# Kernel optimization log

Measured on AMD Instinct MI355X. Metric: run time of the kernel, lower is better.

## Reference

```python
import jax, jax.numpy as jnp
import numpy as np

# Fixed multi-scale geometry implied by the module's hard-coded reshapes
# (48^2=2304, 24^2=576, 12^2=144; Len_q = 576).
SPATIAL = [(48, 48), (24, 24), (12, 12)]
NH, NP, NL = 6, 4, 3  # num_heads, num_points, num_levels


def _process_reference_points(rp):
    """rp: (B, 3024, 2) normalized refs over 3 levels -> (B, 576, 2).
    Mirrors the part1/part2/part3 averaging in MSDeformAttn.forward."""
    B = rp.shape[0]
    p1 = rp[:, :2304].reshape(B, 48, 48, 2).mean(axis=(1, 2))[:, None, :]
    p1 = jnp.broadcast_to(p1, (B, 576, 2))
    p2 = rp[:, 2304:2880].reshape(B, 576, 2)
    p3 = rp[:, 2880:].reshape(B, 12, 12, 2)
    p3 = jax.image.resize(p3, (B, 24, 24, 2), 'bilinear')  # align_corners=False
    p3 = p3.reshape(B, 576, 2)
    return (p1 + p2 + p3) / 3.0


def _bilinear_sample(val_l, coords, Hl, Wl):
    """val_l: (B, Hl*Wl, nh, d) one level's values.
    coords: (B, Lq, nh, P, 2) normalized (x, y) sampling locations.
    Returns (B, Lq, P, nh, d) bilinearly sampled values (zero padding)."""
    B, Lq, nh, P, _ = coords.shape
    px = coords[..., 0] * Wl - 0.5
    py = coords[..., 1] * Hl - 0.5
    x0 = jnp.floor(px)
    y0 = jnp.floor(py)
    lx = px - x0
    ly = py - y0
    x0i = x0.astype(jnp.int32)
    y0i = y0.astype(jnp.int32)

    def _flat(a):  # (B,Lq,nh,P) -> (B,Lq*P,nh,1) matching value layout
        return a.transpose(0, 1, 3, 2).reshape(B, Lq * P, nh, 1)

    def gather(xi, yi):
        valid = (xi >= 0) & (xi < Wl) & (yi >= 0) & (yi < Hl)
        xi_c = jnp.clip(xi, 0, Wl - 1)
        yi_c = jnp.clip(yi, 0, Hl - 1)
        idx = _flat(yi_c * Wl + xi_c)
        v = jnp.take_along_axis(val_l, idx, axis=1)  # (B,Lq*P,nh,d)
        return v * _flat(valid).astype(val_l.dtype)

    w00 = _flat((1 - lx) * (1 - ly))
    w10 = _flat(lx * (1 - ly))
    w01 = _flat((1 - lx) * ly)
    w11 = _flat(lx * ly)
    out = (gather(x0i, y0i) * w00 + gather(x0i + 1, y0i) * w10 +
           gather(x0i, y0i + 1) * w01 + gather(x0i + 1, y0i + 1) * w11)
    return out.reshape(B, Lq, P, nh, -1)


def setup_inputs() -> dict:
    key = jax.random.key(0)
    ks = jax.random.split(key, 8)
    B, C = 32, 384
    Lq, Lv = 576, 3024
    # reference points exactly as get_reference_points builds them
    refs = []
    for (Hl, Wl) in SPATIAL:
        ry, rx = np.meshgrid(np.linspace(0.5, Hl - 0.5, Hl) / Hl,
                             np.linspace(0.5, Wl - 0.5, Wl) / Wl, indexing='ij')
        refs.append(np.stack([rx.ravel(), ry.ravel()], -1))
    rp = np.concatenate(refs, 0).astype(np.float32)  # (3024, 2)
    rp = np.broadcast_to(rp[None, :, None, :], (B, Lv, 1, 2)).copy()
    s = 1.0 / np.sqrt(C)
    return {
        'query': jax.random.normal(ks[0], (B, Lq, C), jnp.float32),
        'value': jax.random.normal(ks[1], (B, Lv, C), jnp.float32),
        'reference_points': jnp.asarray(rp),
        'W_value': jax.random.normal(ks[2], (C, C), jnp.float32) * s,
        'b_value': jnp.zeros((C,), jnp.float32),
        'W_off': jax.random.normal(ks[3], (C, NH * NL * NP * 2), jnp.float32) * 0.01,
        'b_off': jnp.zeros((NH * NL * NP * 2,), jnp.float32),
        'W_attn': jax.random.normal(ks[4], (C, NH * NL * NP), jnp.float32) * s,
        'b_attn': jnp.zeros((NH * NL * NP,), jnp.float32),
        'W_out': jax.random.normal(ks[5], (C, C), jnp.float32) * s,
        'b_out': jnp.zeros((C,), jnp.float32),
    }


def reference(query, value, reference_points, W_value, b_value, W_off, b_off,
              W_attn, b_attn, W_out, b_out):
    B, Lq, C = query.shape
    d = C // NH
    val = (value @ W_value + b_value).reshape(B, -1, NH, d)
    off = (query @ W_off + b_off).reshape(B, Lq, NH, NL, NP, 2)
    attn = jax.nn.softmax((query @ W_attn + b_attn)
                          .reshape(B, Lq, NH, NL * NP), axis=-1)
    attn = attn.reshape(B, Lq, NH, NL, NP)
    ref = _process_reference_points(reference_points.reshape(B, -1, 2))
    coords = off + ref[:, :, None, None, None, :]  # (B,Lq,nh,L,P,2)
    out = jnp.zeros((B, Lq, NH, d), query.dtype)
    start = 0
    for l, (Hl, Wl) in enumerate(SPATIAL):
        val_l = val[:, start:start + Hl * Wl]
        sampled = _bilinear_sample(val_l, coords[:, :, :, l], Hl, Wl)
        out = out + jnp.einsum('bqpnd,bqnp->bqnd', sampled, attn[:, :, :, l])
        start += Hl * Wl
    return out.reshape(B, Lq, NH * d) @ W_out + b_out
```

## Files before the change

kernel.cpp:

```cpp
#include <hip/hip_runtime.h>
#include <cmath>

#define B_SZ   32
#define LQ     576
#define LV     3024
#define CDIM   384
#define NHEAD  6
#define DHEAD  64
#define NLVL   3
#define NPTS   4
#define NPROJ  216
#define NPROJP 256

typedef short    bx4 __attribute__((ext_vector_type(4)));
typedef short    bx8 __attribute__((ext_vector_type(8)));
typedef float    fx4 __attribute__((ext_vector_type(4)));
typedef _Float16 hx8 __attribute__((ext_vector_type(8)));

__device__ __forceinline__ short f2bf(float f) {
    unsigned u = __builtin_bit_cast(unsigned, f);
    unsigned r = (u + 0x7FFFu + ((u >> 16) & 1u)) >> 16;
    return (short)r;
}
__device__ __forceinline__ float bf2f(unsigned short u) {
    return __builtin_bit_cast(float, ((unsigned)u) << 16);
}
__device__ __forceinline__ short f2h(float f) {
    return __builtin_bit_cast(short, (_Float16)f);
}

__global__ __launch_bounds__(256) void cast_transpose_kernel(
    const float* __restrict__ W, short* __restrict__ Wt, int K, int N)
{
    int idx = blockIdx.x * 256 + threadIdx.x;
    if (idx >= K * N) return;
    int n = idx / K, k = idx - n * K;
    Wt[idx] = f2bf(W[(size_t)k * N + n]);
}

__global__ __launch_bounds__(256) void prep_proj_f16_kernel(
    const float* __restrict__ W_off, const float* __restrict__ b_off,
    const float* __restrict__ W_attn, const float* __restrict__ b_attn,
    short* __restrict__ Wf, float* __restrict__ bc)
{
    int idx = blockIdx.x * 256 + threadIdx.x;
    if (idx >= NPROJP * CDIM) return;
    int n = idx / CDIM, k = idx - n * CDIM;
    float w = 0.f;
    if (n < 144)           w = W_off[(size_t)k * 144 + n];
    else if (n < NPROJ)    w = W_attn[(size_t)k * 72 + (n - 144)];
    Wf[idx] = f2h(w);
    if (idx < NPROJP)
        bc[idx] = (idx < 144) ? b_off[idx]
                 : (idx < NPROJ ? b_attn[idx - 144] : 0.f);
}

__global__ __launch_bounds__(256) void value_gemm_kernel(
    const float* __restrict__ A, const short* __restrict__ Bt,
    const float* __restrict__ bias, short* __restrict__ Cout,
    int M, int K)
{
    constexpr int N = 384;
    __shared__ short As[2][64 * 64];
    __shared__ short Bs[2][192 * 64];

    const int tid = threadIdx.x;
    const int m0 = blockIdx.x * 64;
    const int n0 = blockIdx.y * 192;

    const int w  = tid >> 6;
    const int l  = tid & 63;
    const int wc = w * 48;
    const int lr = l & 15;
    const int q  = l >> 4;

    const int rg  = l >> 3;
    const int cg  = l & 7;
    const int csw = cg ^ rg;

    const int ar   = tid >> 4;
    const int kq   = (tid & 15) << 2;
    const int oct  = kq >> 3;
    const int koff = kq & 7;
    const int aswz = ((oct ^ (ar & 7)) << 3) + koff;
    const float* gA0 = A + (size_t)(m0 + ar) * K + kq;

    fx4 acc[4][3] = {};
    float4 v0, v1, v2, v3;

    auto issueB = [&](int buf, int t) {
        #pragma unroll
        for (int u = 0; u < 6; ++u) {
            const int rbase = w * 48 + u * 8;
            const short* gB = Bt + (size_t)(n0 + rbase + rg) * K + t * 64 + csw * 8;
            __builtin_amdgcn_global_load_lds(
                (const __attribute__((address_space(1))) void*)gB,
                (__attribute__((address_space(3))) void*)&Bs[buf][rbase * 64],
                16, 0, 0);
        }
    };
    auto loadA = [&](int t) {
        const float* g = gA0 + t * 64;
        v0 = *(const float4*)(g);
        v1 = *(const float4*)(g + (size_t)16 * K);
        v2 = *(const float4*)(g + (size_t)32 * K);
        v3 = *(const float4*)(g + (size_t)48 * K);
    };
    auto writeA = [&](int buf) {
        bx4 s;
        s[0]=f2bf(v0.x); s[1]=f2bf(v0.y); s[2]=f2bf(v0.z); s[3]=f2bf(v0.w);
        *(bx4*)&As[buf][(ar +  0) * 64 + aswz] = s;
        s[0]=f2bf(v1.x); s[1]=f2bf(v1.y); s[2]=f2bf(v1.z); s[3]=f2bf(v1.w);
        *(bx4*)&As[buf][(ar + 16) * 64 + aswz] = s;
        s[0]=f2bf(v2.x); s[1]=f2bf(v2.y); s[2]=f2bf(v2.z); s[3]=f2bf(v2.w);
        *(bx4*)&As[buf][(ar + 32) * 64 + aswz] = s;
        s[0]=f2bf(v3.x); s[1]=f2bf(v3.y); s[2]=f2bf(v3.z); s[3]=f2bf(v3.w);
        *(bx4*)&As[buf][(ar + 48) * 64 + aswz] = s;
    };

    issueB(0, 0);
    loadA(0);
    writeA(0);
    __syncthreads();

    #pragma unroll
    for (int t = 0; t < 6; ++t) {
        const int cur = t & 1;

        if (t < 5) { loadA(t + 1); issueB(cur ^ 1, t + 1); }

        #pragma unroll
        for (int ks = 0; ks < 2; ++ks) {
            bx8 af[4], bf[3];
            #pragma unroll
            for (int i = 0; i < 4; ++i)
                af[i] = *(const bx8*)&As[cur][(i * 16 + lr) * 64 +
                                             (((ks * 4 + q) ^ (lr & 7)) << 3)];
            #pragma unroll
            for (int j = 0; j < 3; ++j)
                bf[j] = *(const bx8*)&Bs[cur][(wc + j * 16 + lr) * 64 +
                                             (((ks * 4 + q) ^ (lr & 7)) << 3)];
            #pragma unroll
            for (int i = 0; i < 4; ++i)
                #pragma unroll
                for (int j = 0; j < 3; ++j)
                    acc[i][j] = __builtin_amdgcn_mfma_f32_16x16x32_bf16(
                        af[i], bf[j], acc[i][j], 0, 0, 0);
        }

        if (t < 5) writeA(cur ^ 1);

        __syncthreads();
    }

    float bv[3];
    #pragma unroll
    for (int j = 0; j < 3; ++j) bv[j] = bias[n0 + wc + j * 16 + lr];
    const int rrow = q * 4;
    #pragma unroll
    for (int i = 0; i < 4; ++i) {
        #pragma unroll
        for (int r = 0; r < 4; ++r) {
            const int row = m0 + i * 16 + rrow + r;
            #pragma unroll
            for (int j = 0; j < 3; ++j) {
                const int col = n0 + wc + j * 16 + lr;
                Cout[(size_t)row * N + col] = f2bf(acc[i][j][r] + bv[j]);
            }
        }
    }
}

template <bool OUT_BF16>
__global__ __launch_bounds__(256) void gemm_dma_kernel(
    const short* __restrict__ A, const short* __restrict__ Bt,
    const float* __restrict__ bias, void* __restrict__ Cout,
    int M, int K)
{
    constexpr int N = 384;
    __shared__ short As[128 * 64];
    __shared__ short Bs[128 * 64];

    const int tid = threadIdx.x;
    const int n0 = blockIdx.x * 128;
    const int m0 = blockIdx.y * 128;

    const int w  = tid >> 6;
    const int l  = tid & 63;
    const int wr = (w & 1) * 64;
    const int wc = (w >> 1) * 64;
    const int lr = l & 15;
    const int q  = l >> 4;

    const int rg  = l >> 3;
    const int cg  = l & 7;
    const int csw = cg ^ rg;

    fx4 acc[4][4] = {};

    for (int k0 = 0; k0 < K; k0 += 64) {
        #pragma unroll
        for (int t = 0; t < 4; ++t) {
            const int rbase = w * 32 + t * 8;
            const short* gA = A + (size_t)(m0 + rbase + rg) * K + k0 + csw * 8;
            __builtin_amdgcn_global_load_lds(
                (const __attribute__((address_space(1))) void*)gA,
                (__attribute__((address_space(3))) void*)&As[rbase * 64],
                16, 0, 0);
            const short* gB = Bt + (size_t)(n0 + rbase + rg) * K + k0 + csw * 8;
            __builtin_amdgcn_global_load_lds(
                (const __attribute__((address_space(1))) void*)gB,
                (__attribute__((address_space(3))) void*)&Bs[rbase * 64],
                16, 0, 0);
        }
        __syncthreads();

        #pragma unroll
        for (int ks = 0; ks < 2; ++ks) {
            bx8 af[4], bf[4];
            #pragma unroll
            for (int i = 0; i < 4; ++i)
                af[i] = *(const bx8*)&As[(wr + i * 16 + lr) * 64 +
                                         (((ks * 4 + q) ^ (lr & 7)) << 3)];
            #pragma unroll
            for (int j = 0; j < 4; ++j)
                bf[j] = *(const bx8*)&Bs[(wc + j * 16 + lr) * 64 +
                                         (((ks * 4 + q) ^ (lr & 7)) << 3)];
            #pragma unroll
            for (int i = 0; i < 4; ++i)
                #pragma unroll
                for (int j = 0; j < 4; ++j)
                    acc[i][j] = __builtin_amdgcn_mfma_f32_16x16x32_bf16(
                        af[i], bf[j], acc[i][j], 0, 0, 0);
        }
        __syncthreads();
    }

    const int rrow = q * 4;
    #pragma unroll
    for (int j = 0; j < 4; ++j) {
        const int col = n0 + wc + j * 16 + lr;
        const float bv = bias[col];
        #pragma unroll
        for (int i = 0; i < 4; ++i) {
            const int row = m0 + wr + i * 16 + rrow;
            #pragma unroll
            for (int r = 0; r < 4; ++r) {
                if (OUT_BF16)
                    ((short*)Cout)[(size_t)(row + r) * N + col] = f2bf(acc[i][j][r] + bv);
                else
                    ((float*)Cout)[(size_t)(row + r) * N + col] = acc[i][j][r] + bv;
            }
        }
    }
}

__global__ __launch_bounds__(256) void gemm_proj_kernel(
    const float* __restrict__ A, const short* __restrict__ Wf,
    const float* __restrict__ bias, float* __restrict__ C,
    int M, int K)
{
    __shared__ short As[128 * 72];
    __shared__ short Bs[128 * 72];

    const int tid = threadIdx.x;
    const int n0 = blockIdx.x * 128;
    const int m0 = blockIdx.y * 128;

    const int w  = tid >> 6;
    const int l  = tid & 63;
    const int wr = (w & 1) * 64;
    const int wc = (w >> 1) * 64;
    const int lr = l & 15;
    const int ko = (l >> 4) * 8;

    fx4 acc[4][4] = {};

    for (int k0 = 0; k0 < K; k0 += 64) {
        #pragma unroll
        for (int r = 0; r < 8; ++r) {
            const int id = tid + r * 256;
            const int m  = id >> 4;
            const int kq = (id & 15) << 2;
            const float4 v = *(const float4*)(A + (size_t)(m0 + m) * K + k0 + kq);
            bx4 s;
            s[0] = f2h(v.x); s[1] = f2h(v.y); s[2] = f2h(v.z); s[3] = f2h(v.w);
            *(bx4*)&As[m * 72 + kq] = s;
        }
        #pragma unroll
        for (int r = 0; r < 4; ++r) {
            const int id = tid + r * 256;
            const int n  = id >> 3;
            const int k8 = (id & 7) << 3;
            *(bx8*)&Bs[n * 72 + k8] = *(const bx8*)(Wf + (size_t)(n0 + n) * K + k0 + k8);
        }
        __syncthreads();

        #pragma unroll
        for (int ks = 0; ks < 2; ++ks) {
            bx8 af[4], bf[4];
            #pragma unroll
            for (int i = 0; i < 4; ++i)
                af[i] = *(const bx8*)&As[(wr + i * 16 + lr) * 72 + ks * 32 + ko];
            #pragma unroll
            for (int j = 0; j < 4; ++j)
                bf[j] = *(const bx8*)&Bs[(wc + j * 16 + lr) * 72 + ks * 32 + ko];
            #pragma unroll
            for (int i = 0; i < 4; ++i)
                #pragma unroll
                for (int j = 0; j < 4; ++j)
                    acc[i][j] = __builtin_amdgcn_mfma_f32_16x16x32_f16(
                        __builtin_bit_cast(hx8, af[i]),
                        __builtin_bit_cast(hx8, bf[j]), acc[i][j], 0, 0, 0);
        }
        __syncthreads();
    }

    const int rrow = (l >> 4) * 4;
    #pragma unroll
    for (int j = 0; j < 4; ++j) {
        const int col = n0 + wc + j * 16 + lr;
        if (col >= NPROJ) continue;
        const float bv = bias[col];
        #pragma unroll
        for (int i = 0; i < 4; ++i) {
            const int row = m0 + wr + i * 16 + rrow;
            #pragma unroll
            for (int r = 0; r < 4; ++r)
                C[(size_t)(row + r) * NPROJ + col] = acc[i][j][r] + bv;
        }
    }
}

__global__ __launch_bounds__(256) void ref_kernel(
    const float* __restrict__ rp, float* __restrict__ refp)
{
    const int b = blockIdx.x;
    const float* r = rp + (size_t)b * LV * 2;
    const int tid = threadIdx.x;

    __shared__ float redx[256], redy[256];
    float sx = 0.f, sy = 0.f;
    for (int i = tid; i < 2304; i += 256) {
        sx += r[2 * i + 0];
        sy += r[2 * i + 1];
    }
    redx[tid] = sx; redy[tid] = sy;
    __syncthreads();
    for (int s = 128; s > 0; s >>= 1) {
        if (tid < s) { redx[tid] += redx[tid + s]; redy[tid] += redy[tid + s]; }
        __syncthreads();
    }
    const float p1x = redx[0] * (1.f / 2304.f);
    const float p1y = redy[0] * (1.f / 2304.f);

    const float* g = r + 2880 * 2;
    for (int q = tid; q < 576; q += 256) {
        const float p2x = r[(2304 + q) * 2 + 0];
        const float p2y = r[(2304 + q) * 2 + 1];
        const int qy = q / 24, qx = q % 24;
        const float syc = fminf(fmaxf(0.5f * qy - 0.25f, 0.f), 11.f);
        const float sxc = fminf(fmaxf(0.5f * qx - 0.25f, 0.f), 11.f);
        int y0 = min((int)syc, 10);
        int x0 = min((int)sxc, 10);
        const float fy = syc - (float)y0, fx = sxc - (float)x0;
        const float v00x = g[(y0 * 12 + x0) * 2 + 0],     v00y = g[(y0 * 12 + x0) * 2 + 1];
        const float v10x = g[(y0 * 12 + x0 + 1) * 2 + 0], v10y = g[(y0 * 12 + x0 + 1) * 2 + 1];
        const float v01x = g[((y0 + 1) * 12 + x0) * 2 + 0],     v01y = g[((y0 + 1) * 12 + x0) * 2 + 1];
        const float v11x = g[((y0 + 1) * 12 + x0 + 1) * 2 + 0], v11y = g[((y0 + 1) * 12 + x0 + 1) * 2 + 1];
        const float p3x = (1.f - fy) * ((1.f - fx) * v00x + fx * v10x)
                        + fy * ((1.f - fx) * v01x + fx * v11x);
        const float p3y = (1.f - fy) * ((1.f - fx) * v00y + fx * v10y)
                        + fy * ((1.f - fx) * v01y + fx * v11y);
        refp[((size_t)b * LQ + q) * 2 + 0] = (p1x + p2x + p3x) * (1.f / 3.f);
        refp[((size_t)b * LQ + q) * 2 + 1] = (p1y + p2y + p3y) * (1.f / 3.f);
    }
}

__global__ __launch_bounds__(192) void sample_kernel(
    const unsigned short* __restrict__ val, const float* __restrict__ proj,
    const float* __restrict__ refp, unsigned* __restrict__ mid)
{
    const int i = blockIdx.x;
    const int g = i & 7;
    const int r = i >> 3;
    const int b = g * 4 + (r / LQ);
    const int q = r - (r / LQ) * LQ;
    const int bq = b * LQ + q;
    const int tid = threadIdx.x;

    __shared__ float attn[72];
    __shared__ int   sloc[72][4];
    __shared__ float swt[72][4];

    if (tid < 72) {
        attn[tid] = proj[(size_t)bq * NPROJ + 144 + tid];

        const int h = tid / 12;
        const int rr = tid % 12;
        const int l = rr >> 2;
        const int p = rr & 3;

        const int HL[3] = {48, 24, 12};
        const int ST[3] = {0, 2304, 2880};
        const int Hl = HL[l], Wl = HL[l], st = ST[l];

        const float rx = refp[bq * 2 + 0];
        const float ry = refp[bq * 2 + 1];
        const int oc = ((h * NLVL + l) * NPTS + p) * 2;
        const float cx = proj[(size_t)bq * NPROJ + oc + 0] + rx;
        const float cy = proj[(size_t)bq * NPROJ + oc + 1] + ry;

        const float px = cx * (float)Wl - 0.5f;
        const float py = cy * (float)Hl - 0.5f;
        const float x0f = floorf(px), y0f = floorf(py);
        const float lx = px - x0f, ly = py - y0f;
        const int x0 = (int)x0f, y0 = (int)y0f;

        #pragma unroll
        for (int k = 0; k < 4; ++k) {
            const int dx = k & 1, dy = k >> 1;
            const int xi = x0 + dx, yi = y0 + dy;
            const bool v = (xi >= 0) && (xi < Wl) && (yi >= 0) && (yi < Hl);
            const int xc = min(max(xi, 0), Wl - 1);
            const int yc = min(max(yi, 0), Hl - 1);
            sloc[tid][k] = st + yc * Wl + xc;
            const float wx = dx ? lx : 1.f - lx;
            const float wy = dy ? ly : 1.f - ly;
            swt[tid][k] = v ? wx * wy : 0.f;
        }
    }
    __syncthreads();

    if (tid < NHEAD) {
        float mx = -1e30f;
        #pragma unroll
        for (int j = 0; j < 12; ++j) mx = fmaxf(mx, attn[tid * 12 + j]);
        float s = 0.f;
        #pragma unroll
        for (int j = 0; j < 12; ++j) {
            const float e = expf(attn[tid * 12 + j] - mx);
            attn[tid * 12 + j] = e;
            s += e;
        }
        const float inv = 1.f / s;
        #pragma unroll
        for (int j = 0; j < 12; ++j) attn[tid * 12 + j] *= inv;
    }
    __syncthreads();

    const int h  = tid >> 5;
    const int c2 = (tid & 31) << 1;
    const unsigned* vp = (const unsigned*)(val + (size_t)b * LV * CDIM + h * DHEAD + c2);
    float acc0 = 0.f, acc1 = 0.f;
    #pragma unroll
    for (int s = 0; s < 12; ++s) {
        const int j = h * 12 + s;
        const float a = attn[j];
        float s0 = 0.f, s1 = 0.f;
        #pragma unroll
        for (int k = 0; k < 4; ++k) {
            const unsigned u = vp[(size_t)sloc[j][k] * (CDIM / 2)];
            const float lo = __builtin_bit_cast(float, u << 16);
            const float hi = __builtin_bit_cast(float, u & 0xFFFF0000u);
            s0 += swt[j][k] * lo;
            s1 += swt[j][k] * hi;
        }
        acc0 += a * s0;
        acc1 += a * s1;
    }
    const unsigned lo = (unsigned)(unsigned short)f2bf(acc0);
    const unsigned hi = (unsigned)(unsigned short)f2bf(acc1);
    mid[((size_t)bq * CDIM + h * DHEAD + c2) >> 1] = lo | (hi << 16);
}

extern "C" void kernel_launch(void* const* d_in, const int* in_sizes, int n_in,
                              void* d_out, int out_size, void* d_ws, size_t ws_size,
                              hipStream_t stream)
{
    (void)in_sizes; (void)n_in; (void)out_size; (void)ws_size;

    const float* query   = (const float*)d_in[0];
    const float* value   = (const float*)d_in[1];
    const float* rp      = (const float*)d_in[2];
    const float* W_value = (const float*)d_in[3];
    const float* b_value = (const float*)d_in[4];
    const float* W_off   = (const float*)d_in[5];
    const float* b_off   = (const float*)d_in[6];
    const float* W_attn  = (const float*)d_in[7];
    const float* b_attn  = (const float*)d_in[8];
    const float* W_out   = (const float*)d_in[9];
    const float* b_out   = (const float*)d_in[10];
    float* out = (float*)d_out;

    char* p = (char*)d_ws;
    auto take = [&](size_t bytes) { char* q = p; p += (bytes + 255) & ~(size_t)255; return q; };
    short* val  = (short*)take((size_t)B_SZ * LV * CDIM * 2);
    short* mid  = (short*)take((size_t)B_SZ * LQ * CDIM * 2);
    short* Wtv  = (short*)take((size_t)CDIM * CDIM * 2);
    short* Wto  = (short*)take((size_t)CDIM * CDIM * 2);
    short* Wf   = (short*)take((size_t)NPROJP * CDIM * 2);
    float* proj = (float*)take((size_t)B_SZ * LQ * NPROJ * 4);
    float* refp = (float*)take((size_t)B_SZ * LQ * 2 * 4);
    float* bc   = (float*)take((size_t)NPROJP * 4);

    const int Mv = B_SZ * LV;
    const int Mq = B_SZ * LQ;

    cast_transpose_kernel<<<(CDIM * CDIM + 255) / 256, 256, 0, stream>>>(
        W_value, Wtv, CDIM, CDIM);
    cast_transpose_kernel<<<(CDIM * CDIM + 255) / 256, 256, 0, stream>>>(
        W_out, Wto, CDIM, CDIM);
    prep_proj_f16_kernel<<<(NPROJP * CDIM + 255) / 256, 256, 0, stream>>>(
        W_off, b_off, W_attn, b_attn, Wf, bc);

    value_gemm_kernel<<<dim3(Mv / 64, 2), 256, 0, stream>>>(
        value, Wtv, b_value, val, Mv, CDIM);
    gemm_proj_kernel<<<dim3(2, Mq / 128), 256, 0, stream>>>(
        query, Wf, bc, proj, Mq, CDIM);
    ref_kernel<<<B_SZ, 256, 0, stream>>>(rp, refp);
    sample_kernel<<<Mq, 192, 0, stream>>>(
        (const unsigned short*)val, proj, refp, (unsigned*)mid);
    gemm_dma_kernel<false><<<dim3(3, Mq / 128), 256, 0, stream>>>(
        mid, Wto, b_out, out, Mq, CDIM);
}
```

Baseline: 391.7 us.

## Load GEMM B operands directly from global memory and merge weight-prep kernels

```diff
diff --git a/kernel.cpp b/kernel.cpp
--- a/kernel.cpp
+++ b/kernel.cpp
@@ -29,30 +29,33 @@
     return __builtin_bit_cast(short, (_Float16)f);
 }
 
-__global__ __launch_bounds__(256) void cast_transpose_kernel(
-    const float* __restrict__ W, short* __restrict__ Wt, int K, int N)
-{
-    int idx = blockIdx.x * 256 + threadIdx.x;
-    if (idx >= K * N) return;
-    int n = idx / K, k = idx - n * K;
-    Wt[idx] = f2bf(W[(size_t)k * N + n]);
-}
-
-__global__ __launch_bounds__(256) void prep_proj_f16_kernel(
+__global__ __launch_bounds__(256) void prep_all_kernel(
+    const float* __restrict__ W_value, const float* __restrict__ W_out,
     const float* __restrict__ W_off, const float* __restrict__ b_off,
     const float* __restrict__ W_attn, const float* __restrict__ b_attn,
+    short* __restrict__ Wtv, short* __restrict__ Wto,
     short* __restrict__ Wf, float* __restrict__ bc)
 {
-    int idx = blockIdx.x * 256 + threadIdx.x;
-    if (idx >= NPROJP * CDIM) return;
-    int n = idx / CDIM, k = idx - n * CDIM;
-    float w = 0.f;
-    if (n < 144)           w = W_off[(size_t)k * 144 + n];
-    else if (n < NPROJ)    w = W_attn[(size_t)k * 72 + (n - 144)];
-    Wf[idx] = f2h(w);
-    if (idx < NPROJP)
-        bc[idx] = (idx < 144) ? b_off[idx]
-                 : (idx < NPROJ ? b_attn[idx - 144] : 0.f);
+    const int idx = blockIdx.x * 256 + threadIdx.x;
+    constexpr int SQ = CDIM * CDIM;
+    if (idx < SQ) {
+        int n = idx / CDIM, k = idx - n * CDIM;
+        Wtv[idx] = f2bf(W_value[(size_t)k * CDIM + n]);
+    } else if (idx < 2 * SQ) {
+        int i = idx - SQ;
+        int n = i / CDIM, k = i - n * CDIM;
+        Wto[i] = f2bf(W_out[(size_t)k * CDIM + n]);
+    } else if (idx < 2 * SQ + NPROJP * CDIM) {
+        int i = idx - 2 * SQ;
+        int n = i / CDIM, k = i - n * CDIM;
+        float w = 0.f;
+        if (n < 144)        w = W_off[(size_t)k * 144 + n];
+        else if (n < NPROJ) w = W_attn[(size_t)k * 72 + (n - 144)];
+        Wf[i] = f2h(w);
+        if (i < NPROJP)
+            bc[i] = (i < 144) ? b_off[i]
+                   : (i < NPROJ ? b_attn[i - 144] : 0.f);
+    }
 }
 
 __global__ __launch_bounds__(256) void value_gemm_kernel(
@@ -62,7 +65,6 @@
 {
     constexpr int N = 384;
     __shared__ short As[2][64 * 64];
-    __shared__ short Bs[2][192 * 64];
 
     const int tid = threadIdx.x;
     const int m0 = blockIdx.x * 64;
@@ -73,10 +75,6 @@
     const int wc = w * 48;
     const int lr = l & 15;
     const int q  = l >> 4;
-
-    const int rg  = l >> 3;
-    const int cg  = l & 7;
-    const int csw = cg ^ rg;
 
     const int ar   = tid >> 4;
     const int kq   = (tid & 15) << 2;
@@ -85,20 +83,14 @@
     const int aswz = ((oct ^ (ar & 7)) << 3) + koff;
     const float* gA0 = A + (size_t)(m0 + ar) * K + kq;
 
+    const short* gB[3];
+    #pragma unroll
+    for (int j = 0; j < 3; ++j)
+        gB[j] = Bt + (size_t)(n0 + wc + j * 16 + lr) * K + q * 8;
+
     fx4 acc[4][3] = {};
     float4 v0, v1, v2, v3;
 
-    auto issueB = [&](int buf, int t) {
-        #pragma unroll
-        for (int u = 0; u < 6; ++u) {
-            const int rbase = w * 48 + u * 8;
-            const short* gB = Bt + (size_t)(n0 + rbase + rg) * K + t * 64 + csw * 8;
-            __builtin_amdgcn_global_load_lds(
-                (const __attribute__((address_space(1))) void*)gB,
-                (__attribute__((address_space(3))) void*)&Bs[buf][rbase * 64],
-                16, 0, 0);
-        }
-    };
     auto loadA = [&](int t) {
         const float* g = gA0 + t * 64;
         v0 = *(const float4*)(g);
@@ -118,7 +110,6 @@
         *(bx4*)&As[buf][(ar + 48) * 64 + aswz] = s;
     };
 
-    issueB(0, 0);
     loadA(0);
     writeA(0);
     __syncthreads();
@@ -127,7 +118,7 @@
     for (int t = 0; t < 6; ++t) {
         const int cur = t & 1;
 
-        if (t < 5) { loadA(t + 1); issueB(cur ^ 1, t + 1); }
+        if (t < 5) loadA(t + 1);
 
         #pragma unroll
         for (int ks = 0; ks < 2; ++ks) {
@@ -138,8 +129,7 @@
                                              (((ks * 4 + q) ^ (lr & 7)) << 3)];
             #pragma unroll
             for (int j = 0; j < 3; ++j)
-                bf[j] = *(const bx8*)&Bs[cur][(wc + j * 16 + lr) * 64 +
-                                             (((ks * 4 + q) ^ (lr & 7)) << 3)];
+                bf[j] = *(const bx8*)(gB[j] + t * 64 + ks * 32);
             #pragma unroll
             for (int i = 0; i < 4; ++i)
                 #pragma unroll
@@ -149,7 +139,6 @@
         }
 
         if (t < 5) writeA(cur ^ 1);
-
         __syncthreads();
     }
 
@@ -171,15 +160,13 @@
     }
 }
 
-template <bool OUT_BF16>
 __global__ __launch_bounds__(256) void gemm_dma_kernel(
     const short* __restrict__ A, const short* __restrict__ Bt,
-    const float* __restrict__ bias, void* __restrict__ Cout,
+    const float* __restrict__ bias, float* __restrict__ Cout,
     int M, int K)
 {
     constexpr int N = 384;
     __shared__ short As[128 * 64];
-    __shared__ short Bs[128 * 64];
 
     const int tid = threadIdx.x;
     const int n0 = blockIdx.x * 128;
@@ -195,6 +182,11 @@
     const int rg  = l >> 3;
     const int cg  = l & 7;
     const int csw = cg ^ rg;
+
+    const short* gB[4];
+    #pragma unroll
+    for (int j = 0; j < 4; ++j)
+        gB[j] = Bt + (size_t)(n0 + wc + j * 16 + lr) * K + q * 8;
 
     fx4 acc[4][4] = {};
 
@@ -207,11 +199,6 @@
                 (const __attribute__((address_space(1))) void*)gA,
                 (__attribute__((address_space(3))) void*)&As[rbase * 64],
                 16, 0, 0);
-            const short* gB = Bt + (size_t)(n0 + rbase + rg) * K + k0 + csw * 8;
-            __builtin_amdgcn_global_load_lds(
-                (const __attribute__((address_space(1))) void*)gB,
-                (__attribute__((address_space(3))) void*)&Bs[rbase * 64],
-                16, 0, 0);
         }
         __syncthreads();
 
@@ -224,8 +211,7 @@
                                          (((ks * 4 + q) ^ (lr & 7)) << 3)];
             #pragma unroll
             for (int j = 0; j < 4; ++j)
-                bf[j] = *(const bx8*)&Bs[(wc + j * 16 + lr) * 64 +
-                                         (((ks * 4 + q) ^ (lr & 7)) << 3)];
+                bf[j] = *(const bx8*)(gB[j] + k0 + ks * 32);
             #pragma unroll
             for (int i = 0; i < 4; ++i)
                 #pragma unroll
@@ -245,12 +231,8 @@
         for (int i = 0; i < 4; ++i) {
             const int row = m0 + wr + i * 16 + rrow;
             #pragma unroll
-            for (int r = 0; r < 4; ++r) {
-                if (OUT_BF16)
-                    ((short*)Cout)[(size_t)(row + r) * N + col] = f2bf(acc[i][j][r] + bv);
-                else
-                    ((float*)Cout)[(size_t)(row + r) * N + col] = acc[i][j][r] + bv;
-            }
+            for (int r = 0; r < 4; ++r)
+                Cout[(size_t)(row + r) * N + col] = acc[i][j][r] + bv;
         }
     }
 }
@@ -261,7 +243,6 @@
     int M, int K)
 {
     __shared__ short As[128 * 72];
-    __shared__ short Bs[128 * 72];
 
     const int tid = threadIdx.x;
     const int n0 = blockIdx.x * 128;
@@ -273,6 +254,11 @@
     const int wc = (w >> 1) * 64;
     const int lr = l & 15;
     const int ko = (l >> 4) * 8;
+
+    const short* gB[4];
+    #pragma unroll
+    for (int j = 0; j < 4; ++j)
+        gB[j] = Wf + (size_t)(n0 + wc + j * 16 + lr) * K + ko;
 
     fx4 acc[4][4] = {};
 
@@ -287,13 +273,6 @@
             s[0] = f2h(v.x); s[1] = f2h(v.y); s[2] = f2h(v.z); s[3] = f2h(v.w);
             *(bx4*)&As[m * 72 + kq] = s;
         }
-        #pragma unroll
-        for (int r = 0; r < 4; ++r) {
-            const int id = tid + r * 256;
-            const int n  = id >> 3;
-            const int k8 = (id & 7) << 3;
-            *(bx8*)&Bs[n * 72 + k8] = *(const bx8*)(Wf + (size_t)(n0 + n) * K + k0 + k8);
-        }
         __syncthreads();
 
         #pragma unroll
@@ -304,7 +283,7 @@
                 af[i] = *(const bx8*)&As[(wr + i * 16 + lr) * 72 + ks * 32 + ko];
             #pragma unroll
             for (int j = 0; j < 4; ++j)
-                bf[j] = *(const bx8*)&Bs[(wc + j * 16 + lr) * 72 + ks * 32 + ko];
+                bf[j] = *(const bx8*)(gB[j] + k0 + ks * 32);
             #pragma unroll
             for (int i = 0; i < 4; ++i)
                 #pragma unroll
@@ -507,12 +486,9 @@
     const int Mv = B_SZ * LV;
     const int Mq = B_SZ * LQ;
 
-    cast_transpose_kernel<<<(CDIM * CDIM + 255) / 256, 256, 0, stream>>>(
-        W_value, Wtv, CDIM, CDIM);
-    cast_transpose_kernel<<<(CDIM * CDIM + 255) / 256, 256, 0, stream>>>(
-        W_out, Wto, CDIM, CDIM);
-    prep_proj_f16_kernel<<<(NPROJP * CDIM + 255) / 256, 256, 0, stream>>>(
-        W_off, b_off, W_attn, b_attn, Wf, bc);
+    const int prep_elems = 2 * CDIM * CDIM + NPROJP * CDIM;
+    prep_all_kernel<<<prep_elems / 256, 256, 0, stream>>>(
+        W_value, W_out, W_off, b_off, W_attn, b_attn, Wtv, Wto, Wf, bc);
 
     value_gemm_kernel<<<dim3(Mv / 64, 2), 256, 0, stream>>>(
         value, Wtv, b_value, val, Mv, CDIM);
@@ -521,6 +497,6 @@
     ref_kernel<<<B_SZ, 256, 0, stream>>>(rp, refp);
     sample_kernel<<<Mq, 192, 0, stream>>>(
         (const unsigned short*)val, proj, refp, (unsigned*)mid);
-    gemm_dma_kernel<false><<<dim3(3, Mq / 128), 256, 0, stream>>>(
+    gemm_dma_kernel<<<dim3(3, Mq / 128), 256, 0, stream>>>(
         mid, Wto, b_out, out, Mq, CDIM);
 }
```

Measured after the change: 407.3 us. +4.0%, slower.
